# Kernel optimization log

Measured on AMD Instinct MI355X. Metric: run time of the kernel, lower is better.

Reference implementation:

```python
import jax, jax.numpy as jnp
import numpy as np

B, Q, K, QS, KS, H, DV = 16, 128, 512, 256, 256, 128, 256


def setup_inputs() -> dict:
    key = jax.random.key(0)
    ks = jax.random.split(key, 7)
    return {
        "queries": jax.random.normal(ks[0], (B, Q, QS), dtype=jnp.float32),
        "keys": jax.random.normal(ks[1], (B, K, KS), dtype=jnp.float32),
        "values": jax.random.normal(ks[2], (B, K, DV), dtype=jnp.float32),
        "valid_lens": jax.random.randint(ks[3], (B,), 1, K + 1),
        # Linear weights (no bias); stored as [in, hidden] so x @ W == nn.Linear
        "W_q": jax.random.normal(ks[4], (QS, H), dtype=jnp.float32) / np.float32(np.sqrt(QS)),
        "W_k": jax.random.normal(ks[5], (KS, H), dtype=jnp.float32) / np.float32(np.sqrt(KS)),
        "w_v": jax.random.normal(ks[6], (H,), dtype=jnp.float32) / np.float32(np.sqrt(H)),
    }


def reference(queries, keys, values, valid_lens, W_q, W_k, w_v):
    # Projections
    q = jnp.einsum('bqd,dh->bqh', queries, W_q)   # [B,Q,H]
    k = jnp.einsum('bkd,dh->bkh', keys, W_k)      # [B,K,H]
    # Additive (Bahdanau) score: tanh(q + k) . w_v  -> [B,Q,K]
    feats = jnp.tanh(q[:, :, None, :] + k[:, None, :, :])  # [B,Q,K,H] big intermediate
    scores = jnp.einsum('bqkh,h->bqk', feats, w_v)
    # masked softmax over keys: positions >= valid_len get -1e6 (as in torch ref)
    mask = jnp.arange(K)[None, None, :] < valid_lens[:, None, None]  # [B,1,K] bcast
    scores = jnp.where(mask, scores, jnp.float32(-1e6))
    attn = jax.nn.softmax(scores, axis=-1)        # [B,Q,K]
    # dropout p=0.0 -> identity
    return jnp.einsum('bqk,bkd->bqd', attn, values)  # [B,Q,DV]
```

## Files before the change

### kernel.cpp

```cpp
#include <hip/hip_runtime.h>
#include <hip/hip_bf16.h>

#define NB 16
#define NQ 128
#define NK 512
#define DIN 256
#define NH 128
#define NDV 256

#define CSC 2.8853900817779268f

__global__ __launch_bounds__(256) void proj_both_kernel(
    const float* __restrict__ Q, const float* __restrict__ K,
    const float* __restrict__ Wq, const float* __restrict__ Wk,
    float* __restrict__ QP, float* __restrict__ KPT)
{
    __shared__ float Xl[16 * DIN];
    __shared__ float Wl[64 * NH];
    const int tid = threadIdx.x;
    int blk = blockIdx.x;
    const float *X, *W;
    int b, r0, isq;
    if (blk < 128) { isq = 1; b = blk >> 3; r0 = (blk & 7) * 16;
                     X = Q + ((size_t)b * NQ + r0) * DIN; W = Wq; }
    else { blk -= 128; isq = 0; b = blk >> 5; r0 = (blk & 31) * 16;
           X = K + ((size_t)b * NK + r0) * DIN; W = Wk; }

    {
        const float4* Xg = (const float4*)X;
        float4* Xs = (float4*)Xl;
        #pragma unroll
        for (int i = 0; i < 4; ++i) Xs[tid + 256 * i] = Xg[tid + 256 * i];
    }

    const int h  = tid & 127;
    const int rg = tid >> 7;
    float acc[8];
    #pragma unroll
    for (int r = 0; r < 8; ++r) acc[r] = 0.f;

    for (int dc = 0; dc < 4; ++dc) {
        __syncthreads();
        {
            const float4* Wg = (const float4*)(W + dc * 64 * NH);
            float4* Ws = (float4*)Wl;
            #pragma unroll
            for (int i = 0; i < 8; ++i) Ws[tid + 256 * i] = Wg[tid + 256 * i];
        }
        __syncthreads();
        #pragma unroll 4
        for (int d = 0; d < 64; d += 4) {
            float w0 = Wl[(d + 0) * NH + h];
            float w1 = Wl[(d + 1) * NH + h];
            float w2 = Wl[(d + 2) * NH + h];
            float w3 = Wl[(d + 3) * NH + h];
            #pragma unroll
            for (int r = 0; r < 8; ++r) {
                float4 x = *(const float4*)&Xl[(rg * 8 + r) * DIN + dc * 64 + d];
                acc[r] += x.x * w0 + x.y * w1 + x.z * w2 + x.w * w3;
            }
        }
    }
    if (isq) {
        float* Pp = QP + ((size_t)(b * NQ + r0 + rg * 8)) * NH + h;
        #pragma unroll
        for (int r = 0; r < 8; ++r) Pp[(size_t)r * NH] = acc[r] * CSC;
    } else {
        float* Pp = KPT + ((size_t)b * NH + h) * NK + r0 + rg * 8;
        float4 o0, o1;
        o0.x = acc[0]*CSC; o0.y = acc[1]*CSC; o0.z = acc[2]*CSC; o0.w = acc[3]*CSC;
        o1.x = acc[4]*CSC; o1.y = acc[5]*CSC; o1.z = acc[6]*CSC; o1.w = acc[7]*CSC;
        *(float4*)Pp = o0; *(float4*)(Pp + 4) = o1;
    }
}

__global__ __launch_bounds__(256) void attn_fused_kernel(
    const float* __restrict__ QP, const float* __restrict__ KPT,
    const float* __restrict__ wv, const int* __restrict__ vlen,
    const float* __restrict__ V, float* __restrict__ OUT)
{
    __shared__ float qcl[4 * NH];
    __shared__ float wvl[NH];
    __shared__ float sc[4][NK];
    __shared__ float part[4][4][NDV];
    const int tid = threadIdx.x;
    const int b  = blockIdx.x >> 5;
    const int q0 = (blockIdx.x & 31) * 4;

    {
        const float* qg = QP + ((size_t)b * NQ + q0) * NH;
        qcl[tid] = qg[tid];
        qcl[tid + 256] = qg[tid + 256];
        if (tid < NH) wvl[tid] = -2.0f * wv[tid];
    }
    __syncthreads();

    int vl = vlen[b];
    vl = vl < 1 ? 1 : (vl > NK ? NK : vl);

    {
        const int k1 = tid, k2 = tid + 256;
        const float* kb = KPT + (size_t)b * NH * NK;
        float a[8];
        #pragma unroll
        for (int i = 0; i < 8; ++i) a[i] = 0.f;
        #pragma unroll 4
        for (int h = 0; h < NH; ++h) {
            float kv1 = kb[(size_t)h * NK + k1];
            float kv2 = kb[(size_t)h * NK + k2];
            float wq  = wvl[h];
            #pragma unroll
            for (int r = 0; r < 4; ++r) {
                float qv = qcl[r * NH + h];
                float t1 = __builtin_amdgcn_exp2f(qv + kv1);
                float t2 = __builtin_amdgcn_exp2f(qv + kv2);
                a[r]     += wq * __builtin_amdgcn_rcpf(t1 + 1.0f);
                a[r + 4] += wq * __builtin_amdgcn_rcpf(t2 + 1.0f);
            }
        }
        const bool v1 = (k1 < vl), v2 = (k2 < vl);
        #pragma unroll
        for (int r = 0; r < 4; ++r) {
            sc[r][k1] = v1 ? a[r]     : -1e6f;
            sc[r][k2] = v2 ? a[r + 4] : -1e6f;
        }
    }
    __syncthreads();

    const int w = tid >> 6, lane = tid & 63;
    {
        float vals[8];
        float m = -3.0e38f;
        #pragma unroll
        for (int i = 0; i < 8; ++i) { vals[i] = sc[w][lane + 64 * i]; m = fmaxf(m, vals[i]); }
        #pragma unroll
        for (int off = 32; off; off >>= 1) m = fmaxf(m, __shfl_xor(m, off, 64));
        float s = 0.f;
        #pragma unroll
        for (int i = 0; i < 8; ++i) {
            vals[i] = __builtin_amdgcn_exp2f((vals[i] - m) * 1.4426950408889634f);
            s += vals[i];
        }
        #pragma unroll
        for (int off = 32; off; off >>= 1) s += __shfl_xor(s, off, 64);
        const float invs = 1.0f / s;
        #pragma unroll
        for (int i = 0; i < 8; ++i) sc[w][lane + 64 * i] = vals[i] * invs;
    }
    __syncthreads();

    {
        float4 o[4];
        #pragma unroll
        for (int r = 0; r < 4; ++r) { o[r].x = 0.f; o[r].y = 0.f; o[r].z = 0.f; o[r].w = 0.f; }
        const float* vb = V + (size_t)b * NK * NDV + lane * 4;
        const int kbase = w * 128;
        #pragma unroll 4
        for (int kk = 0; kk < 128; ++kk) {
            const int k = kbase + kk;
            float4 v4 = *(const float4*)(vb + (size_t)k * NDV);
            float p0 = sc[0][k], p1 = sc[1][k], p2 = sc[2][k], p3 = sc[3][k];
            o[0].x += p0 * v4.x; o[0].y += p0 * v4.y; o[0].z += p0 * v4.z; o[0].w += p0 * v4.w;
            o[1].x += p1 * v4.x; o[1].y += p1 * v4.y; o[1].z += p1 * v4.z; o[1].w += p1 * v4.w;
            o[2].x += p2 * v4.x; o[2].y += p2 * v4.y; o[2].z += p2 * v4.z; o[2].w += p2 * v4.w;
            o[3].x += p3 * v4.x; o[3].y += p3 * v4.y; o[3].z += p3 * v4.z; o[3].w += p3 * v4.w;
        }
        #pragma unroll
        for (int r = 0; r < 4; ++r)
            *(float4*)&part[w][r][lane * 4] = o[r];
    }
    __syncthreads();
    {
        const int r = tid >> 6, d4 = tid & 63;
        float4 p0 = *(const float4*)&part[0][r][d4 * 4];
        float4 p1 = *(const float4*)&part[1][r][d4 * 4];
        float4 p2 = *(const float4*)&part[2][r][d4 * 4];
        float4 p3 = *(const float4*)&part[3][r][d4 * 4];
        float4 s;
        s.x = (p0.x + p1.x) + (p2.x + p3.x);
        s.y = (p0.y + p1.y) + (p2.y + p3.y);
        s.z = (p0.z + p1.z) + (p2.z + p3.z);
        s.w = (p0.w + p1.w) + (p2.w + p3.w);
        *(float4*)&OUT[((size_t)b * NQ + q0 + r) * NDV + d4 * 4] = s;
    }
}

extern "C" void kernel_launch(void* const* d_in, const int* in_sizes, int n_in,
                              void* d_out, int out_size, void* d_ws, size_t ws_size,
                              hipStream_t stream) {
    const float* queries = (const float*)d_in[0];
    const float* keys    = (const float*)d_in[1];
    const float* values  = (const float*)d_in[2];
    const int*   vlen    = (const int*)d_in[3];
    const float* Wq      = (const float*)d_in[4];
    const float* Wk      = (const float*)d_in[5];
    const float* wv      = (const float*)d_in[6];
    float* out           = (float*)d_out;

    float* qp  = (float*)d_ws;
    float* kpt = qp + (size_t)NB * NQ * NH;

    proj_both_kernel<<<128 + 512, 256, 0, stream>>>(queries, keys, Wq, Wk, qp, kpt);
    attn_fused_kernel<<<NB * 32, 256, 0, stream>>>(qp, kpt, wv, vlen, values, out);
}
```

Baseline: 146.0 us.

## Split projection into smaller blocks and double attention block threads

```diff
diff --git a/kernel.cpp b/kernel.cpp
--- a/kernel.cpp
+++ b/kernel.cpp
@@ -15,66 +15,64 @@
     const float* __restrict__ Wq, const float* __restrict__ Wk,
     float* __restrict__ QP, float* __restrict__ KPT)
 {
-    __shared__ float Xl[16 * DIN];
-    __shared__ float Wl[64 * NH];
+    __shared__ float Xl[8 * DIN];
     const int tid = threadIdx.x;
     int blk = blockIdx.x;
-    const float *X, *W;
+    const float* X; const float2* W2;
     int b, r0, isq;
-    if (blk < 128) { isq = 1; b = blk >> 3; r0 = (blk & 7) * 16;
-                     X = Q + ((size_t)b * NQ + r0) * DIN; W = Wq; }
-    else { blk -= 128; isq = 0; b = blk >> 5; r0 = (blk & 31) * 16;
-           X = K + ((size_t)b * NK + r0) * DIN; W = Wk; }
+    if (blk < 256) { isq = 1; b = blk >> 4; r0 = (blk & 15) * 8;
+                     X = Q + ((size_t)b * NQ + r0) * DIN; W2 = (const float2*)Wq; }
+    else { blk -= 256; isq = 0; b = blk >> 6; r0 = (blk & 63) * 8;
+           X = K + ((size_t)b * NK + r0) * DIN; W2 = (const float2*)Wk; }
 
     {
         const float4* Xg = (const float4*)X;
         float4* Xs = (float4*)Xl;
+        Xs[tid] = Xg[tid];
+        Xs[tid + 256] = Xg[tid + 256];
+    }
+    __syncthreads();
+
+    const int h2 = tid & 63;
+    const int rg = tid >> 6;
+    float acc[2][2] = {{0.f, 0.f}, {0.f, 0.f}};
+
+    #pragma unroll 8
+    for (int d = 0; d < DIN; d += 4) {
+        float2 w0 = W2[(d + 0) * 64 + h2];
+        float2 w1 = W2[(d + 1) * 64 + h2];
+        float2 w2 = W2[(d + 2) * 64 + h2];
+        float2 w3 = W2[(d + 3) * 64 + h2];
         #pragma unroll
-        for (int i = 0; i < 4; ++i) Xs[tid + 256 * i] = Xg[tid + 256 * i];
+        for (int r = 0; r < 2; ++r) {
+            float4 x = *(const float4*)&Xl[(rg * 2 + r) * DIN + d];
+            acc[r][0] += x.x * w0.x + x.y * w1.x + x.z * w2.x + x.w * w3.x;
+            acc[r][1] += x.x * w0.y + x.y * w1.y + x.z * w2.y + x.w * w3.y;
+        }
     }
 
-    const int h  = tid & 127;
-    const int rg = tid >> 7;
-    float acc[8];
-    #pragma unroll
-    for (int r = 0; r < 8; ++r) acc[r] = 0.f;
-
-    for (int dc = 0; dc < 4; ++dc) {
+    if (isq) {
+        #pragma unroll
+        for (int r = 0; r < 2; ++r) {
+            float2 o; o.x = acc[r][0] * CSC; o.y = acc[r][1] * CSC;
+            *(float2*)&QP[((size_t)b * NQ + r0 + rg * 2 + r) * NH + 2 * h2] = o;
+        }
+    } else {
+        float* T = Xl;
         __syncthreads();
-        {
-            const float4* Wg = (const float4*)(W + dc * 64 * NH);
-            float4* Ws = (float4*)Wl;
-            #pragma unroll
-            for (int i = 0; i < 8; ++i) Ws[tid + 256 * i] = Wg[tid + 256 * i];
+        #pragma unroll
+        for (int r = 0; r < 2; ++r) {
+            T[(2 * h2 + 0) * 12 + rg * 2 + r] = acc[r][0] * CSC;
+            T[(2 * h2 + 1) * 12 + rg * 2 + r] = acc[r][1] * CSC;
         }
         __syncthreads();
-        #pragma unroll 4
-        for (int d = 0; d < 64; d += 4) {
-            float w0 = Wl[(d + 0) * NH + h];
-            float w1 = Wl[(d + 1) * NH + h];
-            float w2 = Wl[(d + 2) * NH + h];
-            float w3 = Wl[(d + 3) * NH + h];
-            #pragma unroll
-            for (int r = 0; r < 8; ++r) {
-                float4 x = *(const float4*)&Xl[(rg * 8 + r) * DIN + dc * 64 + d];
-                acc[r] += x.x * w0 + x.y * w1 + x.z * w2 + x.w * w3;
-            }
-        }
-    }
-    if (isq) {
-        float* Pp = QP + ((size_t)(b * NQ + r0 + rg * 8)) * NH + h;
-        #pragma unroll
-        for (int r = 0; r < 8; ++r) Pp[(size_t)r * NH] = acc[r] * CSC;
-    } else {
-        float* Pp = KPT + ((size_t)b * NH + h) * NK + r0 + rg * 8;
-        float4 o0, o1;
-        o0.x = acc[0]*CSC; o0.y = acc[1]*CSC; o0.z = acc[2]*CSC; o0.w = acc[3]*CSC;
-        o1.x = acc[4]*CSC; o1.y = acc[5]*CSC; o1.z = acc[6]*CSC; o1.w = acc[7]*CSC;
-        *(float4*)Pp = o0; *(float4*)(Pp + 4) = o1;
+        const int h = tid >> 1, half = tid & 1;
+        float4 o = *(const float4*)&T[h * 12 + half * 4];
+        *(float4*)&KPT[((size_t)b * NH + h) * NK + r0 + half * 4] = o;
     }
 }
 
-__global__ __launch_bounds__(256) void attn_fused_kernel(
+__global__ __launch_bounds__(512) void attn_fused_kernel(
     const float* __restrict__ QP, const float* __restrict__ KPT,
     const float* __restrict__ wv, const int* __restrict__ vlen,
     const float* __restrict__ V, float* __restrict__ OUT)
@@ -82,53 +80,44 @@
     __shared__ float qcl[4 * NH];
     __shared__ float wvl[NH];
     __shared__ float sc[4][NK];
-    __shared__ float part[4][4][NDV];
+    __shared__ float part[8][4][NDV];
     const int tid = threadIdx.x;
     const int b  = blockIdx.x >> 5;
     const int q0 = (blockIdx.x & 31) * 4;
 
-    {
-        const float* qg = QP + ((size_t)b * NQ + q0) * NH;
-        qcl[tid] = qg[tid];
-        qcl[tid + 256] = qg[tid + 256];
-        if (tid < NH) wvl[tid] = -2.0f * wv[tid];
-    }
+    qcl[tid] = QP[((size_t)b * NQ + q0) * NH + tid];
+    if (tid < NH) wvl[tid] = -2.0f * wv[tid];
     __syncthreads();
 
     int vl = vlen[b];
     vl = vl < 1 ? 1 : (vl > NK ? NK : vl);
 
     {
-        const int k1 = tid, k2 = tid + 256;
-        const float* kb = KPT + (size_t)b * NH * NK;
-        float a[8];
-        #pragma unroll
-        for (int i = 0; i < 8; ++i) a[i] = 0.f;
+        const float* kb = KPT + (size_t)b * NH * NK + tid;
+        float a0 = 0.f, a1 = 0.f, a2 = 0.f, a3 = 0.f;
         #pragma unroll 4
         for (int h = 0; h < NH; ++h) {
-            float kv1 = kb[(size_t)h * NK + k1];
-            float kv2 = kb[(size_t)h * NK + k2];
-            float wq  = wvl[h];
-            #pragma unroll
-            for (int r = 0; r < 4; ++r) {
-                float qv = qcl[r * NH + h];
-                float t1 = __builtin_amdgcn_exp2f(qv + kv1);
-                float t2 = __builtin_amdgcn_exp2f(qv + kv2);
-                a[r]     += wq * __builtin_amdgcn_rcpf(t1 + 1.0f);
-                a[r + 4] += wq * __builtin_amdgcn_rcpf(t2 + 1.0f);
-            }
+            float kv = kb[(size_t)h * NK];
+            float wq = wvl[h];
+            float e0 = __builtin_amdgcn_exp2f(qcl[0 * NH + h] + kv);
+            float e1 = __builtin_amdgcn_exp2f(qcl[1 * NH + h] + kv);
+            float e2 = __builtin_amdgcn_exp2f(qcl[2 * NH + h] + kv);
+            float e3 = __builtin_amdgcn_exp2f(qcl[3 * NH + h] + kv);
+            a0 += wq * __builtin_amdgcn_rcpf(e0 + 1.0f);
+            a1 += wq * __builtin_amdgcn_rcpf(e1 + 1.0f);
+            a2 += wq * __builtin_amdgcn_rcpf(e2 + 1.0f);
+            a3 += wq * __builtin_amdgcn_rcpf(e3 + 1.0f);
         }
-        const bool v1 = (k1 < vl), v2 = (k2 < vl);
-        #pragma unroll
-        for (int r = 0; r < 4; ++r) {
-            sc[r][k1] = v1 ? a[r]     : -1e6f;
-            sc[r][k2] = v2 ? a[r + 4] : -1e6f;
-        }
+        const bool vld = (tid < vl);
+        sc[0][tid] = vld ? a0 : -1e6f;
+        sc[1][tid] = vld ? a1 : -1e6f;
+        sc[2][tid] = vld ? a2 : -1e6f;
+        sc[3][tid] = vld ? a3 : -1e6f;
     }
     __syncthreads();
 
     const int w = tid >> 6, lane = tid & 63;
-    {
+    if (w < 4) {
         float vals[8];
         float m = -3.0e38f;
         #pragma unroll
@@ -150,37 +139,34 @@
     __syncthreads();
 
     {
-        float4 o[4];
-        #pragma unroll
-        for (int r = 0; r < 4; ++r) { o[r].x = 0.f; o[r].y = 0.f; o[r].z = 0.f; o[r].w = 0.f; }
+        float4 o0 = {0,0,0,0}, o1 = {0,0,0,0}, o2 = {0,0,0,0}, o3 = {0,0,0,0};
         const float* vb = V + (size_t)b * NK * NDV + lane * 4;
-        const int kbase = w * 128;
+        const int kb0 = w * 64;
         #pragma unroll 4
-        for (int kk = 0; kk < 128; ++kk) {
-            const int k = kbase + kk;
+        for (int kk = 0; kk < 64; ++kk) {
+            const int k = kb0 + kk;
             float4 v4 = *(const float4*)(vb + (size_t)k * NDV);
             float p0 = sc[0][k], p1 = sc[1][k], p2 = sc[2][k], p3 = sc[3][k];
-            o[0].x += p0 * v4.x; o[0].y += p0 * v4.y; o[0].z += p0 * v4.z; o[0].w += p0 * v4.w;
-            o[1].x += p1 * v4.x; o[1].y += p1 * v4.y; o[1].z += p1 * v4.z; o[1].w += p1 * v4.w;
-            o[2].x += p2 * v4.x; o[2].y += p2 * v4.y; o[2].z += p2 * v4.z; o[2].w += p2 * v4.w;
-            o[3].x += p3 * v4.x; o[3].y += p3 * v4.y; o[3].z += p3 * v4.z; o[3].w += p3 * v4.w;
+            o0.x += p0 * v4.x; o0.y += p0 * v4.y; o0.z += p0 * v4.z; o0.w += p0 * v4.w;
+            o1.x += p1 * v4.x; o1.y += p1 * v4.y; o1.z += p1 * v4.z; o1.w += p1 * v4.w;
+            o2.x += p2 * v4.x; o2.y += p2 * v4.y; o2.z += p2 * v4.z; o2.w += p2 * v4.w;
+            o3.x += p3 * v4.x; o3.y += p3 * v4.y; o3.z += p3 * v4.z; o3.w += p3 * v4.w;
         }
-        #pragma unroll
-        for (int r = 0; r < 4; ++r)
-            *(float4*)&part[w][r][lane * 4] = o[r];
+        *(float4*)&part[w][0][lane * 4] = o0;
+        *(float4*)&part[w][1][lane * 4] = o1;
+        *(float4*)&part[w][2][lane * 4] = o2;
+        *(float4*)&part[w][3][lane * 4] = o3;
     }
     __syncthreads();
-    {
+
+    if (tid < 256) {
         const int r = tid >> 6, d4 = tid & 63;
-        float4 p0 = *(const float4*)&part[0][r][d4 * 4];
-        float4 p1 = *(const float4*)&part[1][r][d4 * 4];
-        float4 p2 = *(const float4*)&part[2][r][d4 * 4];
-        float4 p3 = *(const float4*)&part[3][r][d4 * 4];
-        float4 s;
-        s.x = (p0.x + p1.x) + (p2.x + p3.x);
-        s.y = (p0.y + p1.y) + (p2.y + p3.y);
-        s.z = (p0.z + p1.z) + (p2.z + p3.z);
-        s.w = (p0.w + p1.w) + (p2.w + p3.w);
+        float4 s = {0, 0, 0, 0};
+        #pragma unroll
+        for (int p = 0; p < 8; ++p) {
+            float4 q = *(const float4*)&part[p][r][d4 * 4];
+            s.x += q.x; s.y += q.y; s.z += q.z; s.w += q.w;
+        }
         *(float4*)&OUT[((size_t)b * NQ + q0 + r) * NDV + d4 * 4] = s;
     }
 }
@@ -200,6 +186,6 @@
     float* qp  = (float*)d_ws;
     float* kpt = qp + (size_t)NB * NQ * NH;
 
-    proj_both_kernel<<<128 + 512, 256, 0, stream>>>(queries, keys, Wq, Wk, qp, kpt);
-    attn_fused_kernel<<<NB * 32, 256, 0, stream>>>(qp, kpt, wv, vlen, values, out);
+    proj_both_kernel<<<256 + 1024, 256, 0, stream>>>(queries, keys, Wq, Wk, qp, kpt);
+    attn_fused_kernel<<<NB * 32, 512, 0, stream>>>(qp, kpt, wv, vlen, values, out);
 }
```

Result: slower. 156.4 us (+7.1%).
